# Performance work log

Hardware: AMD Instinct MI355X
Metric: run time of the kernel (lower is better)

## Reference

```python
import jax, jax.numpy as jnp
import numpy as np
from jax import lax

MU = 0.1          # cfg MODEL.MU (FISTA step size)
LMBD = 0.1        # cfg MODEL.LAMBDA[0]
N_STEPS = 4       # cfg MODEL.NUM_LAYERS (unrolled FISTA iterations)
BN_EPS = 1e-5


def _norm_w(W):
    # DictBlock w_norm: each dictionary filter normalized to unit L2 norm.
    # torch does this under no_grad (in-place on .data), so the norm is a constant.
    n = jnp.sqrt(jnp.sum(W * W, axis=(1, 2, 3), keepdims=True))
    return W / lax.stop_gradient(n + 1e-12)


def _conv(x, W, stride, pad):
    return lax.conv_general_dilated(x, W, (stride, stride), [(pad, pad)] * 2,
                                    dimension_numbers=('NCHW', 'OIHW', 'NCHW'))


def _conv_t(z, W, stride, pad, out_pad):
    # torch conv_transpose2d(z, W, stride, padding=pad, output_padding=out_pad)
    k = W.shape[2]
    Wt = jnp.transpose(jnp.flip(W, (2, 3)), (1, 0, 2, 3))  # (in_ch, dict, k, k)
    p = k - 1 - pad
    return lax.conv_general_dilated(z, Wt, (1, 1), [(p, p + out_pad)] * 2,
                                    lhs_dilation=(stride, stride),
                                    dimension_numbers=('NCHW', 'OIHW', 'NCHW'))


def _shrink(c):
    # non-negative soft threshold: relu(c - lmbd*step)
    return jax.nn.relu(c - LMBD * MU)


def _dict_conv(x, W, stride):
    # Unrolled FISTA sparse coding: min_c 0.5||x - W^T c||^2 + lmbd||c||_1, c>=0
    W = _norm_w(W)
    out_pad = stride - 1
    c = _shrink(MU * _conv(x, W, stride, 1))
    c_pre = jnp.zeros_like(c)
    t = 1.0
    for _ in range(N_STEPS - 1):
        t_next = (1.0 + float(np.sqrt(1.0 + 4.0 * t * t))) / 2.0
        a = c + ((t - 1.0) / t_next) * (c - c_pre)
        c_pre = c
        r = x - _conv_t(a, W, stride, 1, out_pad)       # reconstruction residual
        c = _shrink(a + MU * _conv(r, W, stride, 1))    # proximal gradient step
        t = t_next
    return c


def _bn(x, g, b, m, v):
    # eval-mode BatchNorm2d with running stats
    scale = g * lax.rsqrt(v + BN_EPS)
    return (x - m[None, :, None, None]) * scale[None, :, None, None] + b[None, :, None, None]


def setup_inputs() -> dict:
    key = jax.random.key(0)
    ks = jax.random.split(key, 12)
    N, Cin, Cout, H = 32, 128, 256, 56
    x = jax.random.normal(ks[0], (N, Cin, H, H), jnp.float32)
    def unit_norm(W):
        return W / (jnp.sqrt(jnp.sum(W * W, axis=(1, 2, 3), keepdims=True)) + 1e-12)
    W1 = unit_norm(jax.random.normal(ks[1], (Cout, Cin, 3, 3), jnp.float32))
    W2 = unit_norm(jax.random.normal(ks[2], (Cout, Cout, 3, 3), jnp.float32))
    Wsc = jax.random.normal(ks[3], (Cout, Cin, 1, 1), jnp.float32) * 0.05
    def bn(k):
        k1, k2, k3, k4 = jax.random.split(k, 4)
        g = 1.0 + 0.1 * jax.random.normal(k1, (Cout,), jnp.float32)
        b = 0.1 * jax.random.normal(k2, (Cout,), jnp.float32)
        m = 0.1 * jax.random.normal(k3, (Cout,), jnp.float32)
        v = 0.5 + jax.random.uniform(k4, (Cout,), jnp.float32)
        return g, b, m, v
    bn1_g, bn1_b, bn1_m, bn1_v = bn(ks[4])
    bn2_g, bn2_b, bn2_m, bn2_v = bn(ks[5])
    bnsc_g, bnsc_b, bnsc_m, bnsc_v = bn(ks[6])
    return dict(x=x, W1=W1, W2=W2, Wsc=Wsc,
                bn1_g=bn1_g, bn1_b=bn1_b, bn1_m=bn1_m, bn1_v=bn1_v,
                bn2_g=bn2_g, bn2_b=bn2_b, bn2_m=bn2_m, bn2_v=bn2_v,
                bnsc_g=bnsc_g, bnsc_b=bnsc_b, bnsc_m=bnsc_m, bnsc_v=bnsc_v)


def reference(x, W1, W2, Wsc,
              bn1_g, bn1_b, bn1_m, bn1_v,
              bn2_g, bn2_b, bn2_m, bn2_v,
              bnsc_g, bnsc_b, bnsc_m, bnsc_v):
    out = _bn(_dict_conv(x, W1, 2), bn1_g, bn1_b, bn1_m, bn1_v)
    out = _bn(_dict_conv(out, W2, 1), bn2_g, bn2_b, bn2_m, bn2_v)
    sc = _bn(_conv(x, Wsc, 2, 0), bnsc_g, bnsc_b, bnsc_m, bnsc_v)
    return jax.nn.relu(out + sc)
```

## Files before the change

kernel.cpp:

```cpp
#include <hip/hip_runtime.h>
#include <math.h>

#define MU_F 0.1f
#define SHRINK_F 0.01f
#define BN_EPS_F 1e-5f

typedef _Float16 half_t;
typedef _Float16 half8 __attribute__((ext_vector_type(8)));
typedef float f32x4 __attribute__((ext_vector_type(4)));

__device__ __forceinline__ void gll16(const half_t* g, half_t* l) {
    __builtin_amdgcn_global_load_lds(
        (const __attribute__((address_space(1))) void*)g,
        (__attribute__((address_space(3))) void*)l, 16, 0, 0);
}

#define VM_WAIT_BARRIER(N) do {                                   \
    asm volatile("s_waitcnt vmcnt(" #N ")" ::: "memory");         \
    __builtin_amdgcn_s_barrier();                                 \
    __builtin_amdgcn_sched_barrier(0);                            \
} while (0)

template<int KS, int S, int PAD, int MODE>
__global__ __launch_bounds__(512)
void conv_big(const half_t* __restrict__ Ag, const half_t* __restrict__ Xh,
              float* __restrict__ outF, half_t* __restrict__ outH,
              const half_t* __restrict__ auxH, const float* __restrict__ auxF,
              int CA, int Cout, int Hin, int Win, int Hout, int Wout, int ptiles,
              float alpha, float beta, float delta, int relu1,
              const float* __restrict__ pscale, const float* __restrict__ pbias,
              const float* __restrict__ aux3, int relu2,
              const half_t* __restrict__ zpg, int edge_defer,
              float* __restrict__ out2F)
{
    constexpr bool HALO = (KS == 3 && S == 1);
    __shared__ __align__(16) half_t sm[32768];

    const int tid = threadIdx.x;
    const int wv = tid >> 6, ln = tid & 63;
    const int co0 = blockIdx.y * 128;
    const int wco = (wv & 1) * 64, wpx = (wv >> 1) * 32;
    (void)ptiles;

    int bx;
    {
        const int nwg = gridDim.x;
        const int q = nwg >> 3, r8 = nwg & 7;
        const int xcd = blockIdx.x & 7, idx = blockIdx.x >> 3;
        bx = (xcd < r8 ? xcd * (q + 1) : r8 * (q + 1) + (xcd - r8) * q) + idx;
    }
    const int p0 = bx * 128;

    const int PHW1 = Hout * Wout;
    const int NPX  = PHW1 * 32;

    const int fr = ln & 15, q8 = ln >> 4;
    const int sx = (q8 ^ ((fr >> 1) & 3)) << 3;

    const int cpt   = CA >> 5;
    const int total = KS * KS * cpt;

    int eph[2], epw[2], en2[2];
#pragma unroll
    for (int t2 = 0; t2 < 2; ++t2) {
        int px = p0 + wpx + t2 * 16 + fr;
        en2[t2] = px / PHW1; int rem = px - en2[t2] * PHW1;
        eph[t2] = rem / Wout; epw[t2] = rem - eph[t2] * Wout;
    }

    auto issueA = [&](int flat, int slot) {
        const int row = tid >> 2;
        const int ssw = ((tid & 3) ^ ((row >> 1) & 3)) << 3;
        gll16(Ag + ((size_t)flat * Cout + co0 + row) * 32 + ssw,
              sm + slot * 4096 + tid * 8);
    };

    f32x4 acc[4][2] = {};

    if constexpr (HALO) {
        auto issueH = [&](int cc, int hslot) {
            half_t* hb = sm + 16384 + hslot * 8192;
            const int c0 = cc << 5;
#pragma unroll
            for (int p = 0; p < 2; ++p) {
                const int hrow = (tid >> 2) + p * 128;
                const int hpx = p0 - 48 + hrow;
                const int ssw = ((tid & 3) ^ ((hrow >> 1) & 3)) << 3;
                const half_t* src = ((unsigned)hpx < (unsigned)NPX)
                    ? Xh + (size_t)hpx * CA + c0 + ssw : zpg;
                gll16(src, hb + p * 4096 + tid * 8);
            }
        };

        issueH(0, 0);
        issueA(0, 0); issueA(1, 1); issueA(2, 2);
        VM_WAIT_BARRIER(2);

        int f = 0;
        for (int cc = 0; cc < cpt; ++cc) {
            half_t* hb = sm + 16384 + (cc & 1) * 8192;
            for (int ti = 0; ti < 9; ++ti, ++f) {
                half_t* ab = sm + (f & 3) * 4096;
                if (f + 3 < total) issueA(f + 3, (f + 3) & 3);
                const bool moreH = (ti == 4) && (cc + 1 < cpt);
                if (moreH) issueH(cc + 1, (cc + 1) & 1);

                const int kh = (ti * 11) >> 5, kw = ti - 3 * kh;
                const int dh = (MODE == 0) ? kh - 1 : 1 - kh;
                const int dw = (MODE == 0) ? kw - 1 : 1 - kw;
                const int doff = dh * Win + dw;

                half8 fa[4], fb[2];
#pragma unroll
                for (int m = 0; m < 4; ++m)
                    fa[m] = *(const half8*)(ab + (wco + m * 16 + fr) * 32 + sx);
#pragma unroll
                for (int t2 = 0; t2 < 2; ++t2) {
                    const int hidx = wpx + t2 * 16 + fr + 48 + doff;
                    half8 v = *(const half8*)(hb + hidx * 32 +
                                 ((q8 ^ ((hidx >> 1) & 3)) << 3));
                    bool ok = (unsigned)(eph[t2] + dh) < (unsigned)Hin &&
                              (unsigned)(epw[t2] + dw) < (unsigned)Win;
                    half8 z = {};
                    fb[t2] = ok ? v : z;
                }
#pragma unroll
                for (int m = 0; m < 4; ++m)
#pragma unroll
                    for (int t2 = 0; t2 < 2; ++t2)
                        acc[m][t2] = __builtin_amdgcn_mfma_f32_16x16x32_f16(
                            fa[m], fb[t2], acc[m][t2], 0, 0, 0);

                const int nA = (f + 3 < total) ? 2 : ((f + 2 < total) ? 1 : 0);
                if (ti >= 4 && ti <= 6 && cc + 1 < cpt) VM_WAIT_BARRIER(4);
                else if (nA == 2)                        VM_WAIT_BARRIER(2);
                else if (nA == 1)                        VM_WAIT_BARRIER(1);
                else if (f + 1 < total)                  VM_WAIT_BARRIER(0);
            }
        }
    } else {
        const int brow = tid >> 2;
        int bpx = p0 + brow;
        int bn2 = bpx / PHW1; int brem = bpx - bn2 * PHW1;
        const int bph = brem / Wout, bpw = brem - (brem / Wout) * Wout;
        const size_t bnb = (size_t)bn2 * Hin * Win;

        auto issueB = [&](int flat, int slot) {
            int cc, ti;
            if (KS == 1) { cc = flat; ti = 0; }
            else         { cc = (flat * 57) >> 9; ti = flat - 9 * cc; }
            const int kh = (KS == 3) ? ((ti * 11) >> 5) : 0;
            const int kw = (KS == 3) ? (ti - 3 * kh) : 0;
            const int c0 = cc << 5;
            const int hh = bph * S - PAD + kh, ww2 = bpw * S - PAD + kw;
            const bool ok = (unsigned)hh < (unsigned)Hin &&
                            (unsigned)ww2 < (unsigned)Win;
            const int ssw = ((tid & 3) ^ ((brow >> 1) & 3)) << 3;
            const half_t* src = ok
                ? Xh + (bnb + (size_t)(hh * Win + ww2)) * CA + c0 + ssw : zpg;
            gll16(src, sm + 16384 + slot * 4096 + tid * 8);
        };

        issueA(0, 0); issueB(0, 0);
        issueA(1, 1); issueB(1, 1);
        VM_WAIT_BARRIER(2);

        for (int k = 0; k < total; ++k) {
            half_t* ab = sm + (k % 3) * 4096;
            half_t* bb = sm + 16384 + (k % 3) * 4096;
            if (k + 2 < total) { issueA(k + 2, (k + 2) % 3); issueB(k + 2, (k + 2) % 3); }
            half8 fa[4], fb[2];
#pragma unroll
            for (int m = 0; m < 4; ++m)
                fa[m] = *(const half8*)(ab + (wco + m * 16 + fr) * 32 + sx);
#pragma unroll
            for (int t2 = 0; t2 < 2; ++t2)
                fb[t2] = *(const half8*)(bb + (wpx + t2 * 16 + fr) * 32 + sx);
#pragma unroll
            for (int m = 0; m < 4; ++m)
#pragma unroll
                for (int t2 = 0; t2 < 2; ++t2)
                    acc[m][t2] = __builtin_amdgcn_mfma_f32_16x16x32_f16(
                        fa[m], fb[t2], acc[m][t2], 0, 0, 0);
            if (k + 2 < total)      VM_WAIT_BARRIER(2);
            else if (k + 1 < total) VM_WAIT_BARRIER(0);
        }
    }

#pragma unroll
    for (int t = 0; t < 2; ++t) {
        const int oh = eph[t], ow = epw[t], n2 = en2[t];
        size_t ghwc = ((size_t)(n2 * Hout + oh) * Wout + ow) * Cout;
        bool defer = edge_defer && (oh == 0 || ow == 0);
#pragma unroll
        for (int m = 0; m < 4; ++m) {
#pragma unroll
            for (int rr = 0; rr < 4; ++rr) {
                int co_l = co0 + wco + m * 16 + q8 * 4 + rr;
                size_t fidx = ((size_t)(n2 * Cout + co_l) * Hout + oh) * Wout + ow;
                float av = alpha * acc[m][t][rr];
                if (out2F) out2F[fidx] = av;
                float v = av + delta;
                if (auxH) v += beta * (float)auxH[ghwc + co_l];
                if (auxF) v += beta * auxF[fidx];
                if (!defer) {
                    if (relu1) v = fmaxf(v, 0.f);
                    if (pscale) v = pscale[co_l] * v + pbias[co_l];
                    if (aux3) v += aux3[fidx];
                    if (relu2) v = fmaxf(v, 0.f);
                }
                if (outH) outH[ghwc + co_l] = (half_t)v;
                else      outF[fidx] = v;
            }
        }
    }
}

template<int KT>
__global__ __launch_bounds__(256)
void pack_w(const float* __restrict__ W, half_t* __restrict__ Wh,
            half_t* __restrict__ WTh, int Cin, int Cout, int do_norm)
{
    __shared__ float red[256];
    int co = blockIdx.x, tid = threadIdx.x;
    int CK = Cin * KT;
    const float* w = W + (size_t)co * CK;
    float inv = 1.f;
    if (do_norm) {
        float s = 0.f;
        for (int i = tid; i < CK; i += 256) { float v = w[i]; s += v * v; }
        red[tid] = s; __syncthreads();
        for (int o = 128; o > 0; o >>= 1) {
            if (tid < o) red[tid] += red[tid + o];
            __syncthreads();
        }
        inv = 1.f / (sqrtf(red[0]) + 1e-12f);
    }
    for (int i = tid; i < CK; i += 256) {
        int ci = i / KT, tap = i - ci * KT;
        half_t h = (half_t)(w[i] * inv);
        Wh[(((size_t)(ci >> 5) * KT + tap) * Cout + co) * 32 + (ci & 31)] = h;
        if (WTh) WTh[(((size_t)(co >> 5) * KT + tap) * Cin + ci) * 32 + (co & 31)] = h;
    }
}

__global__ __launch_bounds__(256)
void gram_kernel(const half_t* __restrict__ Wh, half_t* __restrict__ Gp,
                 half_t* __restrict__ ChT, half_t* __restrict__ CwT,
                 half_t* __restrict__ CcT)
{
    __shared__ float Wa[9 * 128];
    int co = blockIdx.x, b = threadIdx.x;
    for (int i = b; i < 9 * 128; i += 256) Wa[i] = (float)Wh[(size_t)co * 9 * 128 + i];
    __syncthreads();
    const half_t* Wb = Wh + (size_t)b * 9 * 128;
    auto dot = [&](int tA, int tB) {
        float s = 0.f;
        for (int c = 0; c < 128; ++c) s += Wa[tA * 128 + c] * (float)Wb[tB * 128 + c];
        return s;
    };
    auto lo = [](int t) { return (t == 2) ? 2 : 0; };
    auto hi = [](int t) { return (t == 1) ? 3 : ((t == 2) ? 3 : 1); };
    for (int th = 0; th < 3; ++th)
        for (int tw = 0; tw < 3; ++tw) {
            float s = 0.f;
            for (int kh = lo(th); kh < hi(th); ++kh)
                for (int kw = lo(tw); kw < hi(tw); ++kw)
                    s += dot(kh * 3 + kw, (kh + 2 - 2 * th) * 3 + (kw + 2 - 2 * tw));
            Gp[(((size_t)(b >> 5) * 9 + th * 3 + tw) * 256 + co) * 32 + (b & 31)] = (half_t)s;
        }
    for (int tw = 0; tw < 3; ++tw) {
        float s = 0.f, s2 = 0.f;
        for (int k = lo(tw); k < hi(tw); ++k) {
            s  += dot(k, k + 2 - 2 * tw);
            s2 += dot(k * 3, (k + 2 - 2 * tw) * 3);
        }
        ChT[((size_t)tw * 256 + b) * 256 + co] = (half_t)s;
        CwT[((size_t)tw * 256 + b) * 256 + co] = (half_t)s2;
    }
    CcT[(size_t)b * 256 + co] = (half_t)dot(0, 0);
}

__global__ __launch_bounds__(256)
void pack_raw(const float* __restrict__ W, half_t* __restrict__ Wr, int CK)
{
    __shared__ float red[256];
    int co = blockIdx.x, tid = threadIdx.x;
    const float* w = W + (size_t)co * CK;
    float s = 0.f;
    for (int i = tid; i < CK; i += 256) { float v = w[i]; s += v * v; }
    red[tid] = s; __syncthreads();
    for (int o = 128; o > 0; o >>= 1) {
        if (tid < o) red[tid] += red[tid + o];
        __syncthreads();
    }
    float inv = 1.f / (sqrtf(red[0]) + 1e-12f);
    for (int i = tid; i < CK; i += 256) {
        int ci = i / 9, tap = i - ci * 9;
        Wr[((size_t)co * 9 + tap) * (CK / 9) + ci] = (half_t)(w[i] * inv);
    }
}

__global__ __launch_bounds__(256)
void edge_fix(const half_t* __restrict__ a, half_t* out,
              const half_t* __restrict__ ChT, const half_t* __restrict__ CwT,
              const half_t* __restrict__ CcT,
              const float* __restrict__ ps, const float* __restrict__ pb)
{
    int i = blockIdx.x, n = blockIdx.y, co = threadIdx.x;
    int oh, ow;
    if (i < 28) { oh = 0; ow = i; } else { oh = i - 27; ow = 0; }
    float corr = 0.f;
    if (oh == 0) {
        for (int kw = 0; kw < 3; ++kw) {
            int pw = ow - 1 + kw;
            if ((unsigned)pw < 28u) {
                const half_t* ap = a + ((size_t)(n * 28 + 0) * 28 + pw) * 256;
                const half_t* cp = ChT + (size_t)kw * 256 * 256 + co;
                for (int b2 = 0; b2 < 256; ++b2)
                    corr += (float)cp[(size_t)b2 * 256] * (float)ap[b2];
            }
        }
    }
    if (ow == 0) {
        for (int kh = 0; kh < 3; ++kh) {
            int ph = oh - 1 + kh;
            if ((unsigned)ph < 28u) {
                const half_t* ap = a + ((size_t)(n * 28 + ph) * 28 + 0) * 256;
                const half_t* cp = CwT + (size_t)kh * 256 * 256 + co;
                for (int b2 = 0; b2 < 256; ++b2)
                    corr += (float)cp[(size_t)b2 * 256] * (float)ap[b2];
            }
        }
    }
    if (oh == 0 && ow == 0) {
        const half_t* ap = a + ((size_t)(n * 28) * 28) * 256;
        for (int b2 = 0; b2 < 256; ++b2)
            corr -= (float)CcT[(size_t)b2 * 256 + co] * (float)ap[b2];
    }
    size_t idx = ((size_t)(n * 28 + oh) * 28 + ow) * 256 + co;
    float v = (float)out[idx] + MU_F * corr;
    v = fmaxf(v, 0.f);
    if (ps) v = ps[co] * v + pb[co];
    out[idx] = (half_t)v;
}

__global__ __launch_bounds__(256)
void tx_kernel(const float* __restrict__ x, half_t* __restrict__ xTh)
{
    __shared__ __align__(16) half_t tl[56 * 136];
    int h = blockIdx.x, n = blockIdx.y, tid = threadIdx.x;
    for (int it = 0; it < 28; ++it) {
        int id = tid + it * 256;
        int c = id / 56, w0 = id - c * 56;
        tl[w0 * 136 + c] = (half_t)x[(((size_t)n * 128 + c) * 56 + h) * 56 + w0];
    }
    __syncthreads();
    if (tid < 224) {
        int w0 = tid >> 2, part = tid & 3;
        size_t base = (((size_t)n * 56 + h) * 56 + w0) * 128 + part * 32;
#pragma unroll
        for (int j = 0; j < 4; ++j)
            *(half8*)(xTh + base + j * 8) = *(const half8*)(tl + w0 * 136 + part * 32 + j * 8);
    }
}

__global__ __launch_bounds__(256)
void comb_kernel(const half_t* __restrict__ c, const half_t* __restrict__ p,
                 half_t* __restrict__ a, float w1, float w2, int n8)
{
    int i = blockIdx.x * 256 + threadIdx.x;
    if (i >= n8) return;
    half8 cv = ((const half8*)c)[i];
    half8 pv = ((const half8*)p)[i];
    half8 rres;
#pragma unroll
    for (int j = 0; j < 8; ++j) rres[j] = (half_t)(w1 * (float)cv[j] + w2 * (float)pv[j]);
    ((half8*)a)[i] = rres;
}

__global__ __launch_bounds__(256)
void bn_prep_kernel(const float* __restrict__ g, const float* __restrict__ b,
                    const float* __restrict__ m, const float* __restrict__ v,
                    float* __restrict__ s, float* __restrict__ t, int C)
{
    int i = blockIdx.x * 256 + threadIdx.x;
    if (i < C) {
        float sc = g[i] * rsqrtf(v[i] + BN_EPS_F);
        s[i] = sc; t[i] = b[i] - m[i] * sc;
    }
}

__global__ __launch_bounds__(128)
void zfill_kernel(half_t* __restrict__ p)
{
    p[threadIdx.x] = (half_t)0.f;
}

extern "C" void kernel_launch(void* const* d_in, const int* in_sizes, int n_in,
                              void* d_out, int out_size, void* d_ws, size_t ws_size,
                              hipStream_t stream)
{
    (void)in_sizes; (void)n_in; (void)out_size;
    const float* x    = (const float*)d_in[0];
    const float* W1   = (const float*)d_in[1];
    const float* W2   = (const float*)d_in[2];
    const float* Wsc  = (const float*)d_in[3];
    const float* bn1g = (const float*)d_in[4];
    const float* bn1b = (const float*)d_in[5];
    const float* bn1m = (const float*)d_in[6];
    const float* bn1v = (const float*)d_in[7];
    const float* bn2g = (const float*)d_in[8];
    const float* bn2b = (const float*)d_in[9];
    const float* bn2m = (const float*)d_in[10];
    const float* bn2v = (const float*)d_in[11];
    const float* bscg = (const float*)d_in[12];
    const float* bscb = (const float*)d_in[13];
    const float* bscm = (const float*)d_in[14];
    const float* bscv = (const float*)d_in[15];

    const size_t NB = (size_t)32 * 256 * 28 * 28;
    const size_t NX = (size_t)32 * 128 * 56 * 56;

    char* base = (char*)d_ws;
    size_t off = 0;
    auto alloc = [&](size_t nbytes) -> void* {
        void* r = base + off;
        off = (off + nbytes + 255) & ~(size_t)255;
        return r;
    };
    half_t* Wh1  = (half_t*)alloc(294912 * 2);
    half_t* Wr1  = (half_t*)alloc(294912 * 2);
    half_t* Wh2  = (half_t*)alloc(589824 * 2);
    half_t* WTh2 = (half_t*)alloc(589824 * 2);
    half_t* Wsch = (half_t*)alloc(32768 * 2);
    half_t* Gph  = (half_t*)alloc(589824 * 2);
    half_t* ChT  = (half_t*)alloc(196608 * 2);
    half_t* CwT  = (half_t*)alloc(196608 * 2);
    half_t* CcT  = (half_t*)alloc(65536 * 2);
    float* bn1s = (float*)alloc(256 * 4);  float* bn1t = (float*)alloc(256 * 4);
    float* bn2s = (float*)alloc(256 * 4);  float* bn2t = (float*)alloc(256 * 4);
    float* bscs = (float*)alloc(256 * 4);  float* bsct = (float*)alloc(256 * 4);
    half_t* zpg  = (half_t*)alloc(256);
    half_t* xTh  = (half_t*)alloc(NX * 2);
    half_t* Pa   = (half_t*)alloc(NB * 2);
    half_t* Pb   = (half_t*)alloc(NB * 2);
    half_t* Pc   = (half_t*)alloc(NB * 2);
    half_t* Py   = (half_t*)alloc(NB * 2);
    half_t* r28h = (half_t*)alloc(NB * 2);
    float*  scF  = (float*)alloc(NB * 4);
    if (off > ws_size) return;

    float*  cxF = (float*)Py;
    half_t* Pd  = (half_t*)xTh;

    float* outp = (float*)d_out;

    double t = 1.0; float al[3];
    for (int i = 0; i < 3; ++i) {
        double tn = (1.0 + sqrt(1.0 + 4.0 * t * t)) / 2.0;
        al[i] = (float)((t - 1.0) / tn); t = tn;
    }

    const dim3 blk(256);
    const dim3 cblk(512);
    const dim3 gB(196, 2, 1);
    const dim3 gE(55, 32, 1);
    const int n8 = (int)(NB / 8);
    const dim3 gC((n8 + 255) / 256);
    const float* NF = nullptr;
    const half_t* NH = nullptr;
    float* NFo = nullptr;
    half_t* NHo = nullptr;

    pack_w<9><<<256, blk, 0, stream>>>(W1, Wh1, nullptr, 128, 256, 1);
    pack_raw<<<256, blk, 0, stream>>>(W1, Wr1, 128 * 9);
    pack_w<9><<<256, blk, 0, stream>>>(W2, Wh2, WTh2, 256, 256, 1);
    pack_w<1><<<256, blk, 0, stream>>>(Wsc, Wsch, nullptr, 128, 256, 0);
    gram_kernel<<<256, blk, 0, stream>>>(Wr1, Gph, ChT, CwT, CcT);
    bn_prep_kernel<<<1, blk, 0, stream>>>(bn1g, bn1b, bn1m, bn1v, bn1s, bn1t, 256);
    bn_prep_kernel<<<1, blk, 0, stream>>>(bn2g, bn2b, bn2m, bn2v, bn2s, bn2t, 256);
    bn_prep_kernel<<<1, blk, 0, stream>>>(bscg, bscb, bscm, bscv, bscs, bsct, 256);
    zfill_kernel<<<1, dim3(128), 0, stream>>>(zpg);
    tx_kernel<<<dim3(56, 32), blk, 0, stream>>>(x, xTh);

    conv_big<3,2,1,0><<<gB, cblk, 0, stream>>>(Wh1, xTh, NFo, Pa, NH, NF,
        128, 256, 56, 56, 28, 28, 196, MU_F, 0.f, -SHRINK_F, 1, NF, NF, NF, 0, zpg, 0, cxF);
    conv_big<1,2,0,0><<<gB, cblk, 0, stream>>>(Wsch, xTh, scF, NHo, NH, NF,
        128, 256, 56, 56, 28, 28, 196, 1.f, 0.f, 0.f, 0, bscs, bsct, NF, 0, zpg, 0, NFo);

    conv_big<3,1,1,0><<<gB, cblk, 0, stream>>>(Gph, Pa, NFo, Pb, Pa, cxF,
        256, 256, 28, 28, 28, 28, 196, -MU_F, 1.f, -SHRINK_F, 1, NF, NF, NF, 0, zpg, 1, NFo);
    edge_fix<<<gE, blk, 0, stream>>>(Pa, Pb, ChT, CwT, CcT, NF, NF);

    comb_kernel<<<gC, blk, 0, stream>>>(Pb, Pa, Pc, 1.f + al[1], -al[1], n8);
    conv_big<3,1,1,0><<<gB, cblk, 0, stream>>>(Gph, Pc, NFo, Pa, Pc, cxF,
        256, 256, 28, 28, 28, 28, 196, -MU_F, 1.f, -SHRINK_F, 1, NF, NF, NF, 0, zpg, 1, NFo);
    edge_fix<<<gE, blk, 0, stream>>>(Pc, Pa, ChT, CwT, CcT, NF, NF);

    comb_kernel<<<gC, blk, 0, stream>>>(Pa, Pb, Pc, 1.f + al[2], -al[2], n8);
    conv_big<3,1,1,0><<<gB, cblk, 0, stream>>>(Gph, Pc, NFo, Pb, Pc, cxF,
        256, 256, 28, 28, 28, 28, 196, -MU_F, 1.f, -SHRINK_F, 1, bn1s, bn1t, NF, 0, zpg, 1, NFo);
    edge_fix<<<gE, blk, 0, stream>>>(Pc, Pb, ChT, CwT, CcT, bn1s, bn1t);

    conv_big<3,1,1,0><<<gB, cblk, 0, stream>>>(Wh2, Pb, NFo, Pa, NH, NF,
        256, 256, 28, 28, 28, 28, 196, MU_F, 0.f, -SHRINK_F, 1, NF, NF, NF, 0, zpg, 0, NFo);

    conv_big<3,1,1,1><<<gB, cblk, 0, stream>>>(WTh2, Pa, NFo, r28h, Pb, NF,
        256, 256, 28, 28, 28, 28, 196, -1.f, 1.f, 0.f, 0, NF, NF, NF, 0, zpg, 0, NFo);
    conv_big<3,1,1,0><<<gB, cblk, 0, stream>>>(Wh2, r28h, NFo, Pd, Pa, NF,
        256, 256, 28, 28, 28, 28, 196, MU_F, 1.f, -SHRINK_F, 1, NF, NF, NF, 0, zpg, 0, NFo);

    comb_kernel<<<gC, blk, 0, stream>>>(Pd, Pa, Pc, 1.f + al[1], -al[1], n8);
    conv_big<3,1,1,1><<<gB, cblk, 0, stream>>>(WTh2, Pc, NFo, r28h, Pb, NF,
        256, 256, 28, 28, 28, 28, 196, -1.f, 1.f, 0.f, 0, NF, NF, NF, 0, zpg, 0, NFo);
    conv_big<3,1,1,0><<<gB, cblk, 0, stream>>>(Wh2, r28h, NFo, Pa, Pc, NF,
        256, 256, 28, 28, 28, 28, 196, MU_F, 1.f, -SHRINK_F, 1, NF, NF, NF, 0, zpg, 0, NFo);

    comb_kernel<<<gC, blk, 0, stream>>>(Pa, Pd, Pc, 1.f + al[2], -al[2], n8);
    conv_big<3,1,1,1><<<gB, cblk, 0, stream>>>(WTh2, Pc, NFo, r28h, Pb, NF,
        256, 256, 28, 28, 28, 28, 196, -1.f, 1.f, 0.f, 0, NF, NF, NF, 0, zpg, 0, NFo);
    conv_big<3,1,1,0><<<gB, cblk, 0, stream>>>(Wh2, r28h, outp, NHo, Pc, NF,
        256, 256, 28, 28, 28, 28, 196, MU_F, 1.f, -SHRINK_F, 1, bn2s, bn2t, scF, 1, zpg, 0, NFo);
}
```

Measured before the change: 1.192 ms.

## Process two K-chunks per barrier with a six-slot weight ring in halo conv

The 3x3 stride-1 halo path is restructured to compute two filter-tap chunks between barriers instead of one. The weight ring grows from 4 to 6 LDS slots, and the prefetch runs four chunks ahead so the loads for the next pair are already in flight. MFMA issue is wrapped in s_setprio so matrix work gets priority over other waves. The goal is to halve barrier and wait overhead per chunk and to overlap loads with compute better, at the cost of more LDS and an assumption that total is even.

```diff
diff --git a/kernel.cpp b/kernel.cpp
--- a/kernel.cpp
+++ b/kernel.cpp
@@ -34,7 +34,7 @@
               float* __restrict__ out2F)
 {
     constexpr bool HALO = (KS == 3 && S == 1);
-    __shared__ __align__(16) half_t sm[32768];
+    __shared__ __align__(16) half_t sm[40960];
 
     const int tid = threadIdx.x;
     const int wv = tid >> 6, ln = tid & 63;
@@ -79,7 +79,7 @@
 
     if constexpr (HALO) {
         auto issueH = [&](int cc, int hslot) {
-            half_t* hb = sm + 16384 + hslot * 8192;
+            half_t* hb = sm + 24576 + hslot * 8192;
             const int c0 = cc << 5;
 #pragma unroll
             for (int p = 0; p < 2; ++p) {
@@ -92,51 +92,61 @@
             }
         };
 
+        auto doChunk = [&](int f) {
+            const int cc = (f * 57) >> 9, ti = f - 9 * cc;
+            half_t* ab = sm + (f % 6) * 4096;
+            half_t* hb = sm + 24576 + (cc & 1) * 8192;
+            const int kh = (ti * 11) >> 5, kw = ti - 3 * kh;
+            const int dh = (MODE == 0) ? kh - 1 : 1 - kh;
+            const int dw = (MODE == 0) ? kw - 1 : 1 - kw;
+            const int doff = dh * Win + dw;
+            half8 fa[4], fb[2];
+#pragma unroll
+            for (int m = 0; m < 4; ++m)
+                fa[m] = *(const half8*)(ab + (wco + m * 16 + fr) * 32 + sx);
+#pragma unroll
+            for (int t2 = 0; t2 < 2; ++t2) {
+                const int hidx = wpx + t2 * 16 + fr + 48 + doff;
+                half8 v = *(const half8*)(hb + hidx * 32 +
+                             ((q8 ^ ((hidx >> 1) & 3)) << 3));
+                bool ok = (unsigned)(eph[t2] + dh) < (unsigned)Hin &&
+                          (unsigned)(epw[t2] + dw) < (unsigned)Win;
+                half8 z = {};
+                fb[t2] = ok ? v : z;
+            }
+            __builtin_amdgcn_s_setprio(1);
+#pragma unroll
+            for (int m = 0; m < 4; ++m)
+#pragma unroll
+                for (int t2 = 0; t2 < 2; ++t2)
+                    acc[m][t2] = __builtin_amdgcn_mfma_f32_16x16x32_f16(
+                        fa[m], fb[t2], acc[m][t2], 0, 0, 0);
+            __builtin_amdgcn_s_setprio(0);
+        };
+
         issueH(0, 0);
-        issueA(0, 0); issueA(1, 1); issueA(2, 2);
+        issueA(0, 0); issueA(1, 1); issueA(2, 2); issueA(3, 3);
         VM_WAIT_BARRIER(2);
 
-        int f = 0;
-        for (int cc = 0; cc < cpt; ++cc) {
-            half_t* hb = sm + 16384 + (cc & 1) * 8192;
-            for (int ti = 0; ti < 9; ++ti, ++f) {
-                half_t* ab = sm + (f & 3) * 4096;
-                if (f + 3 < total) issueA(f + 3, (f + 3) & 3);
-                const bool moreH = (ti == 4) && (cc + 1 < cpt);
-                if (moreH) issueH(cc + 1, (cc + 1) & 1);
-
-                const int kh = (ti * 11) >> 5, kw = ti - 3 * kh;
-                const int dh = (MODE == 0) ? kh - 1 : 1 - kh;
-                const int dw = (MODE == 0) ? kw - 1 : 1 - kw;
-                const int doff = dh * Win + dw;
-
-                half8 fa[4], fb[2];
-#pragma unroll
-                for (int m = 0; m < 4; ++m)
-                    fa[m] = *(const half8*)(ab + (wco + m * 16 + fr) * 32 + sx);
-#pragma unroll
-                for (int t2 = 0; t2 < 2; ++t2) {
-                    const int hidx = wpx + t2 * 16 + fr + 48 + doff;
-                    half8 v = *(const half8*)(hb + hidx * 32 +
-                                 ((q8 ^ ((hidx >> 1) & 3)) << 3));
-                    bool ok = (unsigned)(eph[t2] + dh) < (unsigned)Hin &&
-                              (unsigned)(epw[t2] + dw) < (unsigned)Win;
-                    half8 z = {};
-                    fb[t2] = ok ? v : z;
-                }
-#pragma unroll
-                for (int m = 0; m < 4; ++m)
-#pragma unroll
-                    for (int t2 = 0; t2 < 2; ++t2)
-                        acc[m][t2] = __builtin_amdgcn_mfma_f32_16x16x32_f16(
-                            fa[m], fb[t2], acc[m][t2], 0, 0, 0);
-
-                const int nA = (f + 3 < total) ? 2 : ((f + 2 < total) ? 1 : 0);
-                if (ti >= 4 && ti <= 6 && cc + 1 < cpt) VM_WAIT_BARRIER(4);
-                else if (nA == 2)                        VM_WAIT_BARRIER(2);
-                else if (nA == 1)                        VM_WAIT_BARRIER(1);
-                else if (f + 1 < total)                  VM_WAIT_BARRIER(0);
-            }
+        const int npair = total >> 1;
+        for (int p = 0; p < npair; ++p) {
+            const int f0 = 2 * p;
+            int nA = 0;
+            if (f0 + 4 < total) { issueA(f0 + 4, (f0 + 4) % 6); ++nA; }
+            if (f0 + 5 < total) { issueA(f0 + 5, (f0 + 5) % 6); ++nA; }
+            const int cc0 = (f0 * 57) >> 9,       t0 = f0 - 9 * cc0;
+            const int cc1 = ((f0 + 1) * 57) >> 9, t1 = (f0 + 1) - 9 * cc1;
+            bool hIss = false;
+            if (t0 == 4 && cc0 + 1 < cpt) { issueH(cc0 + 1, (cc0 + 1) & 1); hIss = true; }
+            if (t1 == 4 && cc1 + 1 < cpt) { issueH(cc1 + 1, (cc1 + 1) & 1); hIss = true; }
+
+            doChunk(f0);
+            doChunk(f0 + 1);
+
+            if (hIss)               VM_WAIT_BARRIER(4);
+            else if (nA == 2)       VM_WAIT_BARRIER(2);
+            else if (nA == 1)       VM_WAIT_BARRIER(1);
+            else if (p + 1 < npair) VM_WAIT_BARRIER(0);
         }
     } else {
         const int brow = tid >> 2;
```

New measurement: 1.212 ms. No clear change (+1.7%).
